# Kernel optimization log

Measured on AMD Instinct MI355X. Metric: run time of the kernel, lower is better.

## Reference

```python
import jax, jax.numpy as jnp
import numpy as np

B, E, L = 8, 512, 8192
MAX_W = 4          # max_subword_block_width -> widths 1..3
KSIZE = 5          # conv_kernel_size
DS = 2             # downsample_rate


def setup_inputs() -> dict:
    key = jax.random.key(0)
    k0, k1, k2, k3 = jax.random.split(key, 4)
    x = jax.random.normal(k0, (B, E, L), dtype=jnp.float32)
    # Conv1d(E, E, KSIZE): weight [out_ch, in_ch, k], bias [out_ch]
    conv_w = jax.random.normal(k1, (E, E, KSIZE), dtype=jnp.float32) * (1.0 / np.sqrt(E * KSIZE))
    conv_b = jax.random.normal(k2, (E,), dtype=jnp.float32) * 0.01
    # Linear(E, 1, bias=False): stored as vector [E]
    score_w = jax.random.normal(k3, (E,), dtype=jnp.float32) * (1.0 / np.sqrt(E))
    return {"x": x, "conv_w": conv_w, "conv_b": conv_b, "score_w": score_w}


def reference(x, conv_w, conv_b, score_w):
    length = x.shape[-1]  # original length, captured BEFORE the valid conv (as in torch)
    # Pre-GBST conv, VALID padding -> length shrinks by KSIZE-1
    y = jax.lax.conv_general_dilated(
        x, conv_w, window_strides=(1,), padding="VALID",
        dimension_numbers=("NCH", "OIH", "NCH"))
    y = y + conv_b[None, :, None]

    seqs, scs = [], []
    for w in range(1, MAX_W):
        Lc = y.shape[-1]
        pad = (-Lc) % w
        yp = jnp.pad(y, ((0, 0), (0, 0), (0, pad))) if pad else y
        # avg_pool1d(kernel=w, stride=w) == reshape + mean (zero-pad counts in mean, matching torch)
        cand = yp.reshape(yp.shape[0], yp.shape[1], -1, w).mean(-1)  # [B,E,Nb]
        sc = jnp.einsum("ben,e->bn", cand, score_w)                  # [B,Nb]
        rs = jnp.repeat(cand, w, axis=-1)  # [B,E,Nb*w]
        rc = jnp.repeat(sc, w, axis=-1)    # [B,Nb*w]
        Lr = rs.shape[-1]
        if Lr < length:
            rs = jnp.pad(rs, ((0, 0), (0, 0), (0, length - Lr)))
            rc = jnp.pad(rc, ((0, 0), (0, length - Lr)))
        seqs.append(rs[:, :, :length])
        scs.append(rc[:, :length])
    seqs = jnp.stack(seqs, axis=-1)            # [B,E,L,W-1]
    scs = jnp.stack(scs, axis=-1)[:, None]     # [B,1,L,W-1]
    att = jax.nn.softmax(scs, axis=-1)
    out = (seqs * att).sum(-1)                 # [B,E,L]
    # Downsample via avg_pool1d(kernel=DS, stride=DS)
    b, e, l = out.shape
    out = out[:, :, :(l // DS) * DS].reshape(b, e, l // DS, DS).mean(-1)
    return out
```

## Files before the change

kernel.cpp:

```cpp
#include <hip/hip_runtime.h>
#include <math.h>

#define B_    8
#define E_    512
#define L_    8192
#define K_    5
#define LC    8188
#define LOUT  4096
#define XROWS 8200
#define LCP   8208


typedef float  f32x4   __attribute__((ext_vector_type(4)));
typedef float  f32x16  __attribute__((ext_vector_type(16)));
typedef short  s16x4   __attribute__((ext_vector_type(4)));
typedef short  s16x8   __attribute__((ext_vector_type(8)));

__device__ __forceinline__ unsigned short f2bf(float f) {
    union { float f; unsigned u; } v; v.f = f;
    unsigned r = v.u + 0x7FFFu + ((v.u >> 16) & 1u);
    return (unsigned short)(r >> 16);
}
__device__ __forceinline__ float bflo(unsigned u) {
    union { unsigned u; float f; } v; v.u = u << 16; return v.f;
}
__device__ __forceinline__ float bfhi(unsigned u) {
    union { unsigned u; float f; } v; v.u = u & 0xFFFF0000u; return v.f;
}

__global__ __launch_bounds__(256) void wt_kernel(const float* __restrict__ w,
                                                 unsigned short* __restrict__ Wtb) {
    int idx = blockIdx.x * 256 + threadIdx.x;
    if (idx >= E_ * E_ * K_) return;
    int i    = idx & (E_ - 1);
    int rest = idx >> 9;
    int e    = rest & (E_ - 1);
    int k    = rest >> 9;
    Wtb[idx] = f2bf(w[((size_t)e * E_ + i) * K_ + k]);
}

__global__ __launch_bounds__(256) void xt_kernel(const float* __restrict__ x,
                                                 unsigned short* __restrict__ xT) {
    __shared__ float s[64][65];
    const int b  = blockIdx.z;
    const int i0 = blockIdx.y * 64;
    const int t0 = blockIdx.x * 64;
    #pragma unroll
    for (int j = 0; j < 16; ++j) {
        int idx = threadIdx.x + j * 256;
        int r = idx >> 6, c = idx & 63;
        int t = t0 + c;
        s[c][r] = (t < L_) ? x[((size_t)b * E_ + i0 + r) * L_ + t] : 0.f;
    }
    __syncthreads();
    #pragma unroll
    for (int j = 0; j < 4; ++j) {
        int idx = threadIdx.x + j * 256;
        int tt = idx >> 4, ig = (idx & 15) * 4;
        s16x4 v;
        v[0] = (short)f2bf(s[tt][ig + 0]);
        v[1] = (short)f2bf(s[tt][ig + 1]);
        v[2] = (short)f2bf(s[tt][ig + 2]);
        v[3] = (short)f2bf(s[tt][ig + 3]);
        *(s16x4*)&xT[((size_t)b * XROWS + t0 + tt) * E_ + i0 + ig] = v;
    }
}

__global__ __launch_bounds__(256) void zero_aux(unsigned short* __restrict__ yP,
                                                float* __restrict__ zP) {
    int idx = blockIdx.x * 256 + threadIdx.x;
    if (idx < B_ * LCP) zP[idx] = 0.f;
    int i2 = idx - B_ * LCP;
    if (i2 >= 0 && i2 < B_ * E_ * 20) {
        int row = i2 / 20, j = i2 - row * 20;
        int col = (j < 8) ? j : (8 + LC + (j - 8));
        yP[(size_t)row * LCP + col] = 0;
    }
}

__global__ __launch_bounds__(256, 2) void conv_mfma(const unsigned short* __restrict__ xT,
                                                    const unsigned short* __restrict__ Wtb,
                                                    const float* __restrict__ bias,
                                                    const float* __restrict__ sw,
                                                    unsigned short* __restrict__ yP,
                                                    float* __restrict__ zP) {
    __shared__ unsigned short Xs[520][40];
    __shared__ unsigned short Ws[K_][64][40];
    __shared__ float swb[128];

    const int tid  = threadIdx.x;
    const int nt   = blockIdx.x;
    const int b    = nt >> 4;
    const int tb   = (nt & 15) * 512;
    const int e0   = blockIdx.y * 64;
    const int wave = tid >> 6;
    const int lane = tid & 63;
    const int l32  = lane & 31;
    const int hi   = lane >> 5;
    const int wt0  = wave * 128;

    if (tid < 64)       swb[tid] = sw[e0 + tid];
    else if (tid < 128) swb[tid] = bias[e0 + tid - 64];

    f32x16 acc[2][4];
    #pragma unroll
    for (int es = 0; es < 2; ++es)
        #pragma unroll
        for (int ts = 0; ts < 4; ++ts) acc[es][ts] = (f32x16)0.f;

    const unsigned short* xbase = xT + ((size_t)b * XROWS + tb) * E_;

    s16x8 xpf[9];
    s16x8 wpf[5];

    auto load_tile = [&](int i0) {
        #pragma unroll
        for (int j = 0; j < 8; ++j) {
            int idx = tid + j * 256;
            int r = idx >> 2, c = idx & 3;
            xpf[j] = *(const s16x8*)(xbase + (size_t)r * E_ + i0 + c * 8);
        }
        {
            int idx = tid + 2048;
            if (idx < 2080) {
                int r = idx >> 2, c = idx & 3;
                xpf[8] = *(const s16x8*)(xbase + (size_t)r * E_ + i0 + c * 8);
            }
        }
        #pragma unroll
        for (int j = 0; j < 5; ++j) {
            int idx = tid + j * 256;
            int rl = idx >> 2, c = idx & 3;
            int k = rl >> 6, ep = rl & 63;
            wpf[j] = *(const s16x8*)(Wtb + ((size_t)(k * E_ + e0 + ep) * E_ + i0 + c * 8));
        }
    };
    auto store_tile = [&]() {
        #pragma unroll
        for (int j = 0; j < 8; ++j) {
            int idx = tid + j * 256;
            int r = idx >> 2, c = idx & 3;
            *(s16x8*)&Xs[r][c * 8] = xpf[j];
        }
        {
            int idx = tid + 2048;
            if (idx < 2080) {
                int r = idx >> 2, c = idx & 3;
                *(s16x8*)&Xs[r][c * 8] = xpf[8];
            }
        }
        #pragma unroll
        for (int j = 0; j < 5; ++j) {
            int idx = tid + j * 256;
            int rl = idx >> 2, c = idx & 3;
            int k = rl >> 6, ep = rl & 63;
            *(s16x8*)&Ws[k][ep][c * 8] = wpf[j];
        }
    };

    load_tile(0);
    for (int i0 = 0; i0 < E_; i0 += 32) {
        __syncthreads();
        store_tile();
        __syncthreads();
        if (i0 + 32 < E_) load_tile(i0 + 32);

        #pragma unroll
        for (int k = 0; k < K_; ++k) {
            #pragma unroll
            for (int kk = 0; kk < 2; ++kk) {
                const int co = kk * 16 + hi * 8;
                s16x8 a0 = *(const s16x8*)&Ws[k][l32][co];
                s16x8 a1 = *(const s16x8*)&Ws[k][32 + l32][co];
                #pragma unroll
                for (int ts = 0; ts < 4; ++ts) {
                    s16x8 bv = *(const s16x8*)&Xs[wt0 + ts * 32 + l32 + k][co];
                    acc[0][ts] = __builtin_amdgcn_mfma_f32_32x32x16_bf16(a0, bv, acc[0][ts], 0, 0, 0);
                    acc[1][ts] = __builtin_amdgcn_mfma_f32_32x32x16_bf16(a1, bv, acc[1][ts], 0, 0, 0);
                }
            }
        }
    }

    #pragma unroll
    for (int ts = 0; ts < 4; ++ts) {
        const int t = tb + wt0 + ts * 32 + l32;
        const bool tv = (t < LC);
        float zp = 0.f;
        #pragma unroll
        for (int es = 0; es < 2; ++es) {
            #pragma unroll
            for (int reg = 0; reg < 16; ++reg) {
                int er = es * 32 + (reg & 3) + 8 * (reg >> 2) + 4 * hi;
                float v = acc[es][ts][reg] + swb[64 + er];
                if (tv) yP[((size_t)(b * E_ + e0 + er)) * LCP + 8 + t] = f2bf(v);
                zp += swb[er] * v;
            }
        }
        zp += __shfl_xor(zp, 32);
        if (hi == 0 && tv) atomicAdd(&zP[(size_t)b * LCP + 8 + t], zp);
    }
}

__global__ __launch_bounds__(256) void out2_kernel(const unsigned short* __restrict__ yP,
                                                   const float* __restrict__ zP,
                                                   float* __restrict__ out) {
    __shared__ unsigned short ys8[8][1040];
    __shared__ float  zsL[1040];
    __shared__ float2 attA[512];
    __shared__ float2 attB[512];
    __shared__ float  attC[512];
    const int bx  = blockIdx.x;
    const int b   = bx >> 6;
    const int eg  = bx & 63;
    const int d0  = blockIdx.y << 9;
    const int tid = threadIdx.x;

    const unsigned short* ybase = yP + ((size_t)(b * E_ + eg * 8)) * LCP + 2 * d0;
    const float* zbase = zP + (size_t)b * LCP + 2 * d0;

    #pragma unroll
    for (int r = 0; r < 8; ++r) {
        if (tid < 130) {
            s16x8 v = *(const s16x8*)(ybase + (size_t)r * LCP + tid * 8);
            *(s16x8*)&ys8[r][tid * 8] = v;
        }
    }
    for (int c = tid; c < 260; c += 256)
        *(f32x4*)&zsL[c * 4] = *(const f32x4*)(zbase + c * 4);
    __syncthreads();

    for (int dl = tid; dl < 512; dl += 256) {
        int lt = 2 * dl + 6;
        float z0 = zsL[lt + 0], z1 = zsL[lt + 1], z2 = zsL[lt + 2];
        float z3 = zsL[lt + 3], z4 = zsL[lt + 4], z5 = zsL[lt + 5];
        unsigned t  = 2u * (unsigned)(d0 + dl);
        unsigned r3 = t % 3u;
        float a12 = z1 + z2, a34 = z3 + z4;
        float s0 = z0 + a12, s1 = a12 + z3, s2 = z2 + a34, s3 = a34 + z5;
        float S1a = z2, S1b = z3;
        float S2  = 0.5f * (z2 + z3);
        float S3a = ((r3 == 0u) ? s2 : ((r3 == 1u) ? s1 : s0)) * (1.f / 3.f);
        float S3b = ((r3 == 0u) ? s2 : ((r3 == 1u) ? s1 : s3)) * (1.f / 3.f);
        float m0 = fmaxf(S1a, fmaxf(S2, S3a));
        float e1 = __expf(S1a - m0), e2 = __expf(S2 - m0), e3 = __expf(S3a - m0);
        float r0 = 1.f / (e1 + e2 + e3);
        float m1 = fmaxf(S1b, fmaxf(S2, S3b));
        float f1 = __expf(S1b - m1), f2 = __expf(S2 - m1), f3 = __expf(S3b - m1);
        float r1 = 1.f / (f1 + f2 + f3);
        attA[dl] = make_float2(0.5f * e1 * r0, 0.5f * f1 * r1);
        attB[dl] = make_float2(0.25f * (e2 * r0 + f2 * r1), (0.5f / 3.f) * e3 * r0);
        attC[dl] = (0.5f / 3.f) * f3 * r1;
    }
    __syncthreads();

    const int e    = tid >> 5;
    const int l32b = tid & 31;
    float* orow = out + ((size_t)(b * E_ + eg * 8 + e)) * LOUT + d0;
    const unsigned short* yr = &ys8[e][0];
    #pragma unroll
    for (int ii = 0; ii < 16; ++ii) {
        int dl = l32b + 32 * ii;
        unsigned u0 = *(const unsigned*)(yr + 2 * dl + 6);
        unsigned u1 = *(const unsigned*)(yr + 2 * dl + 8);
        unsigned u2 = *(const unsigned*)(yr + 2 * dl + 10);
        float v0 = bflo(u0), v1 = bfhi(u0);
        float v2 = bflo(u1), v3 = bfhi(u1);
        float v4 = bflo(u2), v5 = bfhi(u2);
        unsigned t  = 2u * (unsigned)(d0 + dl);
        unsigned r3 = t % 3u;
        float a12 = v1 + v2, a34 = v3 + v4;
        float s0 = v0 + a12, s1 = a12 + v3, s2 = v2 + a34, s3 = a34 + v5;
        float C3a = (r3 == 0u) ? s2 : ((r3 == 1u) ? s1 : s0);
        float C3b = (r3 == 0u) ? s2 : ((r3 == 1u) ? s1 : s3);
        float2 wA = attA[dl];
        float2 wB = attB[dl];
        float  wC = attC[dl];
        float o = wA.x * v2 + wA.y * v3 + wB.x * (v2 + v3) + wB.y * C3a + wC * C3b;
        orow[dl] = o;
    }
}

extern "C" void kernel_launch(void* const* d_in, const int* in_sizes, int n_in,
                              void* d_out, int out_size, void* d_ws, size_t ws_size,
                              hipStream_t stream) {
    const float* x       = (const float*)d_in[0];
    const float* conv_w  = (const float*)d_in[1];
    const float* conv_b  = (const float*)d_in[2];
    const float* score_w = (const float*)d_in[3];
    float* out = (float*)d_out;

    unsigned short* base = (unsigned short*)d_ws;
    unsigned short* Wtb = base;
    unsigned short* xT  = Wtb + (size_t)K_ * E_ * E_;
    unsigned short* yP  = xT + (size_t)B_ * XROWS * E_;
    float*          zP  = (float*)(yP + (size_t)B_ * E_ * LCP);

    wt_kernel<<<dim3((E_ * E_ * K_ + 255) / 256), 256, 0, stream>>>(conv_w, Wtb);
    xt_kernel<<<dim3(L_ / 64, E_ / 64, B_), 256, 0, stream>>>(x, xT);
    zero_aux<<<dim3((B_ * LCP + B_ * E_ * 20 + 255) / 256), 256, 0, stream>>>(yP, zP);
    conv_mfma<<<dim3(B_ * 16, E_ / 64), 256, 0, stream>>>(xT, Wtb, conv_b, score_w, yP, zP);
    out2_kernel<<<dim3(B_ * 64, LOUT / 512), 256, 0, stream>>>(yP, zP, out);
}
```

Measured before the change: 419.2 us.

## Prepack conv weights in MFMA fragment order and load directly from global

The weight transpose kernel now writes bf16 weights already arranged in per-lane MFMA A-fragment order, so the conv kernel reads A operands straight from global/L2 and drops the shared-memory weight tile. The time tile per block is halved to 256 to cut LDS use and registers, allowing three blocks per CU and twice as many blocks. The x transpose kernel also switches to vectorized float4 loads. In exchange, weight fragments are reread from cache by every block, with no LDS reuse.

After: 512.3 us. +22.2%, slower.

```diff
diff --git a/kernel.cpp b/kernel.cpp
--- a/kernel.cpp
+++ b/kernel.cpp
@@ -29,14 +29,21 @@
 }
 
 __global__ __launch_bounds__(256) void wt_kernel(const float* __restrict__ w,
-                                                 unsigned short* __restrict__ Wtb) {
+                                                 unsigned short* __restrict__ Wp) {
     int idx = blockIdx.x * 256 + threadIdx.x;
     if (idx >= E_ * E_ * K_) return;
-    int i    = idx & (E_ - 1);
-    int rest = idx >> 9;
-    int e    = rest & (E_ - 1);
-    int k    = rest >> 9;
-    Wtb[idx] = f2bf(w[((size_t)e * E_ + i) * K_ + k]);
+    int j    = idx & 7;
+    int lane = (idx >> 3) & 63;
+    int es   = (idx >> 9) & 1;
+    int kk   = (idx >> 10) & 1;
+    int rest = idx >> 11;
+    int k    = rest % 5;
+    int q    = rest / 5;
+    int i0t  = q & 15;
+    int e0t  = q >> 4;
+    int e = e0t * 64 + es * 32 + (lane & 31);
+    int i = i0t * 32 + kk * 16 + (lane >> 5) * 8 + j;
+    Wp[idx] = f2bf(w[((size_t)e * E_ + i) * K_ + k]);
 }
 
 __global__ __launch_bounds__(256) void xt_kernel(const float* __restrict__ x,
@@ -46,11 +53,14 @@
     const int i0 = blockIdx.y * 64;
     const int t0 = blockIdx.x * 64;
     #pragma unroll
-    for (int j = 0; j < 16; ++j) {
+    for (int j = 0; j < 4; ++j) {
         int idx = threadIdx.x + j * 256;
-        int r = idx >> 6, c = idx & 63;
-        int t = t0 + c;
-        s[c][r] = (t < L_) ? x[((size_t)b * E_ + i0 + r) * L_ + t] : 0.f;
+        int r = idx >> 4, c4 = idx & 15;
+        f32x4 v = *(const f32x4*)(x + ((size_t)b * E_ + i0 + r) * L_ + t0 + c4 * 4);
+        s[c4 * 4 + 0][r] = v[0];
+        s[c4 * 4 + 1][r] = v[1];
+        s[c4 * 4 + 2][r] = v[2];
+        s[c4 * 4 + 3][r] = v[3];
     }
     __syncthreads();
     #pragma unroll
@@ -78,83 +88,69 @@
     }
 }
 
-__global__ __launch_bounds__(256, 2) void conv_mfma(const unsigned short* __restrict__ xT,
-                                                    const unsigned short* __restrict__ Wtb,
+__global__ __launch_bounds__(256, 3) void conv_mfma(const unsigned short* __restrict__ xT,
+                                                    const unsigned short* __restrict__ Wp,
                                                     const float* __restrict__ bias,
                                                     const float* __restrict__ sw,
                                                     unsigned short* __restrict__ yP,
                                                     float* __restrict__ zP) {
-    __shared__ unsigned short Xs[520][40];
-    __shared__ unsigned short Ws[K_][64][40];
+    __shared__ unsigned short Xs[264][40];
     __shared__ float swb[128];
 
     const int tid  = threadIdx.x;
     const int nt   = blockIdx.x;
-    const int b    = nt >> 4;
-    const int tb   = (nt & 15) * 512;
-    const int e0   = blockIdx.y * 64;
+    const int b    = nt >> 5;
+    const int tb   = (nt & 31) * 256;
+    const int e0t  = blockIdx.y;
+    const int e0   = e0t * 64;
     const int wave = tid >> 6;
     const int lane = tid & 63;
     const int l32  = lane & 31;
     const int hi   = lane >> 5;
-    const int wt0  = wave * 128;
+    const int wt0  = wave * 64;
 
     if (tid < 64)       swb[tid] = sw[e0 + tid];
     else if (tid < 128) swb[tid] = bias[e0 + tid - 64];
 
-    f32x16 acc[2][4];
+    f32x16 acc[2][2];
     #pragma unroll
     for (int es = 0; es < 2; ++es)
         #pragma unroll
-        for (int ts = 0; ts < 4; ++ts) acc[es][ts] = (f32x16)0.f;
+        for (int ts = 0; ts < 2; ++ts) acc[es][ts] = (f32x16)0.f;
 
     const unsigned short* xbase = xT + ((size_t)b * XROWS + tb) * E_;
-
-    s16x8 xpf[9];
-    s16x8 wpf[5];
+    const unsigned short* wbase = Wp + (size_t)e0t * 163840 + (size_t)lane * 8;
+
+    s16x8 xpf[5];
 
     auto load_tile = [&](int i0) {
         #pragma unroll
-        for (int j = 0; j < 8; ++j) {
+        for (int j = 0; j < 4; ++j) {
             int idx = tid + j * 256;
             int r = idx >> 2, c = idx & 3;
             xpf[j] = *(const s16x8*)(xbase + (size_t)r * E_ + i0 + c * 8);
         }
         {
-            int idx = tid + 2048;
-            if (idx < 2080) {
+            int idx = tid + 1024;
+            if (idx < 1056) {
                 int r = idx >> 2, c = idx & 3;
-                xpf[8] = *(const s16x8*)(xbase + (size_t)r * E_ + i0 + c * 8);
+                xpf[4] = *(const s16x8*)(xbase + (size_t)r * E_ + i0 + c * 8);
             }
-        }
-        #pragma unroll
-        for (int j = 0; j < 5; ++j) {
-            int idx = tid + j * 256;
-            int rl = idx >> 2, c = idx & 3;
-            int k = rl >> 6, ep = rl & 63;
-            wpf[j] = *(const s16x8*)(Wtb + ((size_t)(k * E_ + e0 + ep) * E_ + i0 + c * 8));
         }
     };
     auto store_tile = [&]() {
         #pragma unroll
-        for (int j = 0; j < 8; ++j) {
+        for (int j = 0; j < 4; ++j) {
             int idx = tid + j * 256;
             int r = idx >> 2, c = idx & 3;
             *(s16x8*)&Xs[r][c * 8] = xpf[j];
         }
         {
-            int idx = tid + 2048;
-            if (idx < 2080) {
+            int idx = tid + 1024;
+            if (idx < 1056) {
                 int r = idx >> 2, c = idx & 3;
-                *(s16x8*)&Xs[r][c * 8] = xpf[8];
+                *(s16x8*)&Xs[r][c * 8] = xpf[4];
             }
-        }
-        #pragma unroll
-        for (int j = 0; j < 5; ++j) {
-            int idx = tid + j * 256;
-            int rl = idx >> 2, c = idx & 3;
-            int k = rl >> 6, ep = rl & 63;
-            *(s16x8*)&Ws[k][ep][c * 8] = wpf[j];
         }
     };
 
@@ -165,15 +161,16 @@
         __syncthreads();
         if (i0 + 32 < E_) load_tile(i0 + 32);
 
+        const unsigned short* wfrag = wbase + (size_t)(i0 >> 5) * 10240;
         #pragma unroll
         for (int k = 0; k < K_; ++k) {
             #pragma unroll
             for (int kk = 0; kk < 2; ++kk) {
+                s16x8 a0 = *(const s16x8*)(wfrag + (size_t)(((k * 2 + kk) * 2 + 0) * 512));
+                s16x8 a1 = *(const s16x8*)(wfrag + (size_t)(((k * 2 + kk) * 2 + 1) * 512));
                 const int co = kk * 16 + hi * 8;
-                s16x8 a0 = *(const s16x8*)&Ws[k][l32][co];
-                s16x8 a1 = *(const s16x8*)&Ws[k][32 + l32][co];
                 #pragma unroll
-                for (int ts = 0; ts < 4; ++ts) {
+                for (int ts = 0; ts < 2; ++ts) {
                     s16x8 bv = *(const s16x8*)&Xs[wt0 + ts * 32 + l32 + k][co];
                     acc[0][ts] = __builtin_amdgcn_mfma_f32_32x32x16_bf16(a0, bv, acc[0][ts], 0, 0, 0);
                     acc[1][ts] = __builtin_amdgcn_mfma_f32_32x32x16_bf16(a1, bv, acc[1][ts], 0, 0, 0);
@@ -183,7 +180,7 @@
     }
 
     #pragma unroll
-    for (int ts = 0; ts < 4; ++ts) {
+    for (int ts = 0; ts < 2; ++ts) {
         const int t = tb + wt0 + ts * 32 + l32;
         const bool tv = (t < LC);
         float zp = 0.f;
@@ -291,14 +288,14 @@
     float* out = (float*)d_out;
 
     unsigned short* base = (unsigned short*)d_ws;
-    unsigned short* Wtb = base;
-    unsigned short* xT  = Wtb + (size_t)K_ * E_ * E_;
+    unsigned short* Wp  = base;
+    unsigned short* xT  = Wp + (size_t)K_ * E_ * E_;
     unsigned short* yP  = xT + (size_t)B_ * XROWS * E_;
     float*          zP  = (float*)(yP + (size_t)B_ * E_ * LCP);
 
-    wt_kernel<<<dim3((E_ * E_ * K_ + 255) / 256), 256, 0, stream>>>(conv_w, Wtb);
+    wt_kernel<<<dim3((E_ * E_ * K_ + 255) / 256), 256, 0, stream>>>(conv_w, Wp);
     xt_kernel<<<dim3(L_ / 64, E_ / 64, B_), 256, 0, stream>>>(x, xT);
     zero_aux<<<dim3((B_ * LCP + B_ * E_ * 20 + 255) / 256), 256, 0, stream>>>(yP, zP);
-    conv_mfma<<<dim3(B_ * 16, E_ / 64), 256, 0, stream>>>(xT, Wtb, conv_b, score_w, yP, zP);
+    conv_mfma<<<dim3(B_ * 32, E_ / 64), 256, 0, stream>>>(xT, Wp, conv_b, score_w, yP, zP);
     out2_kernel<<<dim3(B_ * 64, LOUT / 512), 256, 0, stream>>>(yP, zP, out);
 }
```
